# Performance work log

Hardware: AMD Instinct MI355X
Metric: run time of the kernel (lower is better)

## Reference

```python
import jax, jax.numpy as jnp
import numpy as np

N_NODES = 100000
N_EDGES = 1000000
IN_FEATS = 64
HID = 128
NUM_CLASSES = 10


def setup_inputs() -> dict:
    key = jax.random.key(0)
    ks = jax.random.split(key, 8)
    x = jax.random.normal(ks[0], (N_NODES, IN_FEATS), dtype=jnp.float32)
    edge_index = jax.random.randint(ks[1], (2, N_EDGES), 0, N_NODES, dtype=jnp.int64)
    # Glorot-style init scale for weights
    def w(k, fan_in, fan_out):
        s = (2.0 / (fan_in + fan_out)) ** 0.5
        return jax.random.normal(k, (fan_in, fan_out), dtype=jnp.float32) * s
    return {
        "x": x,
        "edge_index": edge_index,
        "W1": w(ks[2], IN_FEATS, HID),
        "b1": jnp.zeros((HID,), dtype=jnp.float32),
        "W2": w(ks[3], HID, HID),
        "b2": jnp.zeros((HID,), dtype=jnp.float32),
        "Wl": w(ks[4], HID, NUM_CLASSES),
        "bl": jnp.zeros((NUM_CLASSES,), dtype=jnp.float32),
    }


def _gcn_conv(x, src, dst, norm, W, b, num_nodes):
    # PyG GCNConv: h = x W, then out_i = sum_{j->i} norm_ij * h_j + b
    h = x @ W  # [N, out]
    msgs = h[src] * norm[:, None]  # gather + scale  [E+N, out]
    out = jax.ops.segment_sum(msgs, dst, num_segments=num_nodes)
    return out + b


def reference(x, edge_index, W1, b1, W2, b2, Wl, bl):
    N = x.shape[0]
    loops = jnp.arange(N, dtype=edge_index.dtype)
    src = jnp.concatenate([edge_index[0], loops])  # source nodes (messages from)
    dst = jnp.concatenate([edge_index[1], loops])  # target nodes (aggregate at)
    # symmetric normalization: deg over targets (includes self-loops)
    deg = jax.ops.segment_sum(jnp.ones(dst.shape, dtype=x.dtype), dst, num_segments=N)
    dinv = jnp.where(deg > 0, jax.lax.rsqrt(deg), 0.0)
    norm = dinv[src] * dinv[dst]  # [E+N]

    h = jax.nn.relu(_gcn_conv(x, src, dst, norm, W1, b1, N))
    h = jax.nn.relu(_gcn_conv(h, src, dst, norm, W2, b2, N))
    return jax.nn.log_softmax(h @ Wl + bl, axis=1)
```

## Files before the change

kernel.cpp:

```cpp
#include <hip/hip_runtime.h>
#include <hip/hip_fp16.h>
#include <math.h>

#define NUM_CLASSES 10

#define BSH 7
#define BSZ 128
#define BCAP 1792
#define NBMAX 1024
#define P1BATCH 4096

typedef _Float16 half8  __attribute__((ext_vector_type(8)));
typedef _Float16 half4t __attribute__((ext_vector_type(4)));
typedef float    floatx4 __attribute__((ext_vector_type(4)));

__global__ __launch_bounds__(256) void prep_kernel(const float* __restrict__ W1,
                                                   const float* __restrict__ W2,
                                                   const float* __restrict__ Wlc,
                                                   _Float16* __restrict__ W1t,
                                                   _Float16* __restrict__ W2t,
                                                   _Float16* __restrict__ Wct,
                                                   int* __restrict__ fill, int nbuck) {
    const int b = blockIdx.x, tid = threadIdx.x;
    if (b == 0) {
        for (int i = tid; i < nbuck; i += 256) fill[i] = 0;
    }
    if (b < 32) {
        int i = b * 256 + tid;
        int k = i >> 7, c = i & 127;
        W1t[c * 72 + k] = (_Float16)W1[i];
    } else if (b < 96) {
        int i = (b - 32) * 256 + tid;
        int k = i >> 7, c = i & 127;
        W2t[c * 136 + k] = (_Float16)W2[i];
    } else {
        for (int i = tid; i < 16 * 136; i += 256) {
            int c = i / 136, k = i - c * 136;
            float v = (c < NUM_CLASSES && k < 128) ? Wlc[k * NUM_CLASSES + c] : 0.0f;
            Wct[i] = (_Float16)v;
        }
    }
}

__global__ __launch_bounds__(256) void csr_p1_kernel(const int* __restrict__ src,
                                                     const int* __restrict__ dst,
                                                     int* __restrict__ bucket_fill,
                                                     unsigned* __restrict__ pairs, int E) {
    __shared__ int hist[NBMAX], base[NBMAX], cur[NBMAX];
    const int tid = threadIdx.x;
    for (int i = tid; i < NBMAX; i += 256) { hist[i] = 0; cur[i] = 0; }
    __syncthreads();
    const int bb = blockIdx.x * P1BATCH;
    unsigned pk[16];
    int bk[16];
    int cnt = 0;
#pragma unroll
    for (int i = 0; i < 16; ++i) {
        int idx = bb + i * 256 + tid;
        if (idx < E) {
            int s = src[idx], d = dst[idx];
            bk[i] = d >> BSH;
            pk[i] = ((unsigned)s << BSH) | (unsigned)(d & (BSZ - 1));
            atomicAdd(&hist[bk[i]], 1);
            cnt = i + 1;
        }
    }
    __syncthreads();
    for (int i = tid; i < NBMAX; i += 256)
        if (hist[i] > 0) base[i] = atomicAdd(&bucket_fill[i], hist[i]);
    __syncthreads();
#pragma unroll
    for (int i = 0; i < 16; ++i) {
        if (i < cnt) {
            int b = bk[i];
            int r = atomicAdd(&cur[b], 1) + base[b];
            if (r < BCAP) pairs[(size_t)b * BCAP + r] = pk[i];
        }
    }
}

__global__ __launch_bounds__(256) void scan_base_kernel(const int* __restrict__ fill,
                                                        int* __restrict__ bbase, int nbuck) {
    __shared__ int s1[256];
    const int tid = threadIdx.x;
    const int i0 = tid * 4;
    int v[4];
#pragma unroll
    for (int j = 0; j < 4; ++j) v[j] = (i0 + j < nbuck) ? fill[i0 + j] : 0;
    int t = v[0] + v[1] + v[2] + v[3];
    s1[tid] = t;
    __syncthreads();
    for (int off = 1; off < 256; off <<= 1) {
        int u = (tid >= off) ? s1[tid - off] : 0;
        __syncthreads();
        s1[tid] += u;
        __syncthreads();
    }
    int run = s1[tid] - t;
#pragma unroll
    for (int j = 0; j < 4; ++j) {
        if (i0 + j < nbuck) { bbase[i0 + j] = run; run += v[j]; }
    }
    if (tid == 255) bbase[nbuck] = s1[255];
}

__global__ __launch_bounds__(256) void csr_p2_kernel(const int* __restrict__ bucket_fill,
                                                     const int* __restrict__ bucket_base,
                                                     const unsigned* __restrict__ pairs,
                                                     const float* __restrict__ x,
                                                     int* __restrict__ rowstart,
                                                     float* __restrict__ dinv,
                                                     int* __restrict__ csr_src,
                                                     __half2* __restrict__ xs_h,
                                                     int N, int nbuck) {
    __shared__ int cnt[BSZ], excl[BSZ], cur[BSZ];
    __shared__ int s1[BSZ];
    const int tid = threadIdx.x;
    const int b = blockIdx.x;
    const int node0 = b << BSH;
    const int nodes_b = min(BSZ, N - node0);

    if (tid < BSZ) { cnt[tid] = 0; cur[tid] = 0; }
    __syncthreads();
    const int bbase = bucket_base[b];
    const int ne = bucket_fill[b];

    const unsigned* bp = pairs + (size_t)b * BCAP;
    for (int i = tid; i < ne; i += 256)
        atomicAdd(&cnt[bp[i] & (BSZ - 1)], 1);
    __syncthreads();
    int c = (tid < BSZ) ? cnt[tid] : 0;
    if (tid < BSZ) s1[tid] = c;
    __syncthreads();
    for (int off = 1; off < BSZ; off <<= 1) {
        int t = (tid < BSZ && tid >= off) ? s1[tid - off] : 0;
        __syncthreads();
        if (tid < BSZ) s1[tid] += t;
        __syncthreads();
    }
    if (tid < BSZ) excl[tid] = s1[tid] - c;
    __syncthreads();

    if (tid < nodes_b) {
        rowstart[node0 + tid] = bbase + excl[tid];
        dinv[node0 + tid] = rsqrtf((float)cnt[tid] + 1.0f);
    }
    if (b == nbuck - 1 && tid == 0) rowstart[N] = bbase + ne;

    for (int i = tid; i < nodes_b * 32; i += 256) {
        int ln = i >> 5;
        float d = rsqrtf((float)cnt[ln] + 1.0f);
        float2 v = ((const float2*)x)[(size_t)node0 * 32 + i];
        xs_h[(size_t)node0 * 32 + i] = __floats2half2_rn(v.x * d, v.y * d);
    }
    for (int i = tid; i < ne; i += 256) {
        unsigned p = bp[i];
        int d = (int)(p & (BSZ - 1));
        int r = atomicAdd(&cur[d], 1);
        csr_src[bbase + excl[d] + r] = (int)(p >> BSH);
    }
}

template <int F>
__global__ __launch_bounds__(256) void gather_h_kernel(const __half2* __restrict__ hs,
                                                       const float* __restrict__ dinv,
                                                       const int* __restrict__ rowstart,
                                                       const int* __restrict__ csr_src,
                                                       __half2* __restrict__ out, int N) {
    constexpr int F2 = F / 2;
    int node = (blockIdx.x * 256 + threadIdx.x) >> 6;
    int lane = threadIdx.x & 63;
    if (node >= N) return;
    int f2 = lane & (F2 - 1);

    int beg = rowstart[node];
    int end = rowstart[node + 1];
    int deg = end - beg;

    float2 self = __half22float2(hs[(size_t)node * F2 + f2]);
    float2 acc;

    if (deg <= 16) {
        int myidx = (lane < deg) ? csr_src[beg + lane] : node;
        float comp = (float)(deg - 15);
        acc.x = self.x * comp;
        acc.y = self.y * comp;
        float2 v[16];
#pragma unroll
        for (int u = 0; u < 16; ++u) {
            int s = __shfl(myidx, u);
            v[u] = __half22float2(hs[(size_t)s * F2 + f2]);
        }
#pragma unroll
        for (int u = 0; u < 16; ++u) { acc.x += v[u].x; acc.y += v[u].y; }
    } else {
        int lim = deg < 64 ? deg : 64;
        int myidx = (lane < lim) ? csr_src[beg + lane] : node;
        int itersUp = (lim + 7) & ~7;
        float comp = (float)(1 - (itersUp - lim));
        acc.x = self.x * comp;
        acc.y = self.y * comp;
        for (int j = 0; j < itersUp; j += 8) {
            int s[8];
#pragma unroll
            for (int u = 0; u < 8; ++u) s[u] = __shfl(myidx, j + u);
            float2 v[8];
#pragma unroll
            for (int u = 0; u < 8; ++u) v[u] = __half22float2(hs[(size_t)s[u] * F2 + f2]);
#pragma unroll
            for (int u = 0; u < 8; ++u) { acc.x += v[u].x; acc.y += v[u].y; }
        }
        for (int j = beg + 64; j < end; ++j) {
            int s = csr_src[j];
            float2 v = __half22float2(hs[(size_t)s * F2 + f2]);
            acc.x += v.x;
            acc.y += v.y;
        }
    }

    if (F == 128 || lane < 32) {
        float d = dinv[node];
        out[(size_t)node * F2 + f2] = __floats2half2_rn(d * acc.x, d * acc.y);
    }
}

template <int K, bool SCALE_OUT>
__global__ __launch_bounds__(256) void gemm_mfma_kernel(const _Float16* __restrict__ In,
                                                        const _Float16* __restrict__ Wt,
                                                        const float* __restrict__ bias,
                                                        const float* __restrict__ dinv,
                                                        _Float16* __restrict__ Out, int N) {
    constexpr int KP = K + 8;
    constexpr int NC = K / 32;
    __shared__ _Float16 Wl[128 * KP];
    __shared__ float bias_s[128];
    const int tid = threadIdx.x;

    for (int i = tid; i < (128 * KP) / 8; i += 256)
        ((floatx4*)Wl)[i] = ((const floatx4*)Wt)[i];
    if (tid < 128) bias_s[tid] = bias[tid];
    __syncthreads();

    const int lane = tid & 63;
    const int wave = tid >> 6;
    const int q = lane >> 4;
    const int l15 = lane & 15;

#pragma unroll
    for (int iter = 0; iter < 2; ++iter) {
        int myrow = blockIdx.x * 128 + iter * 64 + wave * 16 + l15;
        int r = myrow < N ? myrow : N - 1;
        half8 xf[NC];
#pragma unroll
        for (int c = 0; c < NC; ++c)
            xf[c] = *(const half8*)(In + (size_t)r * K + c * 32 + q * 8);
        floatx4 acc[8];
#pragma unroll
        for (int t = 0; t < 8; ++t) acc[t] = (floatx4){0.f, 0.f, 0.f, 0.f};
#pragma unroll
        for (int c = 0; c < NC; ++c) {
#pragma unroll
            for (int t = 0; t < 8; ++t) {
                half8 wf = *(const half8*)(Wl + (t * 16 + l15) * KP + c * 32 + q * 8);
                acc[t] = __builtin_amdgcn_mfma_f32_16x16x32_f16(wf, xf[c], acc[t], 0, 0, 0);
            }
        }
        if (myrow < N) {
            float sc = SCALE_OUT ? dinv[myrow] : 1.0f;
#pragma unroll
            for (int t = 0; t < 8; ++t) {
                int c0 = t * 16 + q * 4;
                floatx4 bv = *(const floatx4*)&bias_s[c0];
                half4t h;
#pragma unroll
                for (int j = 0; j < 4; ++j)
                    h[j] = (_Float16)(sc * fmaxf(acc[t][j] + bv[j], 0.0f));
                *(half4t*)(Out + (size_t)myrow * 128 + c0) = h;
            }
        }
    }
}

__global__ __launch_bounds__(256) void gemm_final_kernel(const _Float16* __restrict__ In,
                                                         const _Float16* __restrict__ Wt,
                                                         const float* __restrict__ bias,
                                                         const _Float16* __restrict__ Wct,
                                                         const float* __restrict__ bl,
                                                         float* __restrict__ out, int N) {
    constexpr int K = 128, KP = 136, NC = 4;
    __shared__ _Float16 Wl[128 * KP];
    __shared__ _Float16 Wc[16 * KP];
    __shared__ float bias_s[128];
    __shared__ float bl_s[16];
    __shared__ _Float16 act_s[4][16 * KP];
    const int tid = threadIdx.x;

    for (int i = tid; i < (128 * KP) / 8; i += 256)
        ((floatx4*)Wl)[i] = ((const floatx4*)Wt)[i];
    for (int i = tid; i < (16 * KP) / 8; i += 256)
        ((floatx4*)Wc)[i] = ((const floatx4*)Wct)[i];
    if (tid < 128) bias_s[tid] = bias[tid];
    if (tid < 16) bl_s[tid] = (tid < NUM_CLASSES) ? bl[tid] : -1e30f;
    __syncthreads();

    const int lane = tid & 63;
    const int wave = tid >> 6;
    const int q = lane >> 4;
    const int l15 = lane & 15;
    _Float16* As = act_s[wave];

    half8 wcf[NC];
#pragma unroll
    for (int c = 0; c < NC; ++c)
        wcf[c] = *(const half8*)(Wc + l15 * KP + c * 32 + q * 8);
    float myclsb[4];
#pragma unroll
    for (int reg = 0; reg < 4; ++reg) myclsb[reg] = bl_s[q * 4 + reg];

#pragma unroll
    for (int iter = 0; iter < 2; ++iter) {
        int rowbase = blockIdx.x * 128 + iter * 64 + wave * 16;
        int myrow = rowbase + l15;
        int r = myrow < N ? myrow : N - 1;
        half8 xf[NC];
#pragma unroll
        for (int c = 0; c < NC; ++c)
            xf[c] = *(const half8*)(In + (size_t)r * K + c * 32 + q * 8);
        floatx4 acc[8];
#pragma unroll
        for (int t = 0; t < 8; ++t) acc[t] = (floatx4){0.f, 0.f, 0.f, 0.f};
#pragma unroll
        for (int c = 0; c < NC; ++c) {
#pragma unroll
            for (int t = 0; t < 8; ++t) {
                half8 wf = *(const half8*)(Wl + (t * 16 + l15) * KP + c * 32 + q * 8);
                acc[t] = __builtin_amdgcn_mfma_f32_16x16x32_f16(wf, xf[c], acc[t], 0, 0, 0);
            }
        }
#pragma unroll
        for (int t = 0; t < 8; ++t) {
            int c0 = t * 16 + q * 4;
            floatx4 bv = *(const floatx4*)&bias_s[c0];
            half4t h;
#pragma unroll
            for (int j = 0; j < 4; ++j)
                h[j] = (_Float16)fmaxf(acc[t][j] + bv[j], 0.0f);
            *(half4t*)&As[l15 * KP + c0] = h;
        }
        floatx4 lg = (floatx4){0.f, 0.f, 0.f, 0.f};
#pragma unroll
        for (int c = 0; c < NC; ++c) {
            half8 af = *(const half8*)(As + l15 * KP + c * 32 + q * 8);
            lg = __builtin_amdgcn_mfma_f32_16x16x32_f16(wcf[c], af, lg, 0, 0, 0);
        }
        if (myrow < N) {
            float v[4];
#pragma unroll
            for (int reg = 0; reg < 4; ++reg) v[reg] = lg[reg] + myclsb[reg];
            float mx = fmaxf(fmaxf(v[0], v[1]), fmaxf(v[2], v[3]));
            mx = fmaxf(mx, __shfl_xor(mx, 16));
            mx = fmaxf(mx, __shfl_xor(mx, 32));
            float sm = expf(v[0] - mx) + expf(v[1] - mx) + expf(v[2] - mx) + expf(v[3] - mx);
            sm += __shfl_xor(sm, 16);
            sm += __shfl_xor(sm, 32);
            float lse = mx + logf(sm);
#pragma unroll
            for (int reg = 0; reg < 4; ++reg) {
                int cls = q * 4 + reg;
                if (cls < NUM_CLASSES)
                    out[(size_t)myrow * NUM_CLASSES + cls] = v[reg] - lse;
            }
        }
    }
}

extern "C" void kernel_launch(void* const* d_in, const int* in_sizes, int n_in,
                              void* d_out, int out_size, void* d_ws, size_t ws_size,
                              hipStream_t stream) {
    const float* x  = (const float*)d_in[0];
    const int*   ei = (const int*)d_in[1];
    const float* W1 = (const float*)d_in[2];
    const float* b1 = (const float*)d_in[3];
    const float* W2 = (const float*)d_in[4];
    const float* b2 = (const float*)d_in[5];
    const float* Wlc = (const float*)d_in[6];
    const float* bl = (const float*)d_in[7];
    float* out = (float*)d_out;

    const int N = in_sizes[0] / 64;
    const int E = in_sizes[1] / 2;
    const int* src = ei;
    const int* dst = ei + E;
    const int nbuck = (N + BSZ - 1) >> BSH;

    char* ws = (char*)d_ws;
    int*      bucket_fill = (int*)(ws + 0);
    int*      rowstart    = (int*)(ws + 4096);
    float*    dinv        = (float*)(ws + 524288);
    _Float16* W1t         = (_Float16*)(ws + 1048576);
    _Float16* W2t         = (_Float16*)(ws + 1069056);
    _Float16* Wct         = (_Float16*)(ws + 1103872);
    int*      bucket_base = (int*)(ws + 1110016);
    unsigned* pairs       = (unsigned*)(ws + 2097152);
    int*      csr_src     = (int*)(ws + 12582912);
    char*     region1     = ws + 16777216;
    char*     region2     = ws + 68157440;
    __half2*  xs_h = (__half2*)region1;
    __half2*  g1h  = (__half2*)(region1 + 13631488);
    __half2*  g2h  = (__half2*)region1;
    __half2*  a1_h = (__half2*)region2;

    const int P1B = (E + P1BATCH - 1) / P1BATCH;
    const int GB  = (N + 127) / 128;
    const int WVB = (N + 3) / 4;

    prep_kernel<<<97, 256, 0, stream>>>(W1, W2, Wlc, W1t, W2t, Wct, bucket_fill, nbuck);
    csr_p1_kernel<<<P1B, 256, 0, stream>>>(src, dst, bucket_fill, pairs, E);
    scan_base_kernel<<<1, 256, 0, stream>>>(bucket_fill, bucket_base, nbuck);
    csr_p2_kernel<<<nbuck, 256, 0, stream>>>(bucket_fill, bucket_base, pairs, x, rowstart,
                                             dinv, csr_src, xs_h, N, nbuck);

    gather_h_kernel<64><<<WVB, 256, 0, stream>>>(xs_h, dinv, rowstart, csr_src, g1h, N);
    gemm_mfma_kernel<64, true><<<GB, 256, 0, stream>>>((const _Float16*)g1h, W1t, b1, dinv,
                                                       (_Float16*)a1_h, N);

    gather_h_kernel<128><<<WVB, 256, 0, stream>>>(a1_h, dinv, rowstart, csr_src, g2h, N);
    gemm_final_kernel<<<GB, 256, 0, stream>>>((const _Float16*)g2h, W2t, b2, Wct, bl, out, N);
}
```

Measured before the change: 226.0 us.

## Fuse neighbor gathers into GEMM kernels and fold bucket scan into CSR pass

Each gather-aggregate pass is merged into the following MFMA GEMM kernel, so aggregated rows go into shared memory instead of making a round trip through global memory. The separate single-block bucket scan is removed; each csr_p2 block now sums the fills of all preceding buckets itself with a block reduction. This drops two intermediate buffers and three launches. In exchange, gather latency and the GEMM now serialize within a block, and the second fused kernel uses 64-row tiles, so the weight loads into shared memory are repeated twice as often.

Measured after the change: 290.4 us. 1.29x slower.

```diff
diff --git a/kernel.cpp b/kernel.cpp
--- a/kernel.cpp
+++ b/kernel.cpp
@@ -79,33 +79,7 @@
     }
 }
 
-__global__ __launch_bounds__(256) void scan_base_kernel(const int* __restrict__ fill,
-                                                        int* __restrict__ bbase, int nbuck) {
-    __shared__ int s1[256];
-    const int tid = threadIdx.x;
-    const int i0 = tid * 4;
-    int v[4];
-#pragma unroll
-    for (int j = 0; j < 4; ++j) v[j] = (i0 + j < nbuck) ? fill[i0 + j] : 0;
-    int t = v[0] + v[1] + v[2] + v[3];
-    s1[tid] = t;
-    __syncthreads();
-    for (int off = 1; off < 256; off <<= 1) {
-        int u = (tid >= off) ? s1[tid - off] : 0;
-        __syncthreads();
-        s1[tid] += u;
-        __syncthreads();
-    }
-    int run = s1[tid] - t;
-#pragma unroll
-    for (int j = 0; j < 4; ++j) {
-        if (i0 + j < nbuck) { bbase[i0 + j] = run; run += v[j]; }
-    }
-    if (tid == 255) bbase[nbuck] = s1[255];
-}
-
 __global__ __launch_bounds__(256) void csr_p2_kernel(const int* __restrict__ bucket_fill,
-                                                     const int* __restrict__ bucket_base,
                                                      const unsigned* __restrict__ pairs,
                                                      const float* __restrict__ x,
                                                      int* __restrict__ rowstart,
@@ -114,16 +88,24 @@
                                                      __half2* __restrict__ xs_h,
                                                      int N, int nbuck) {
     __shared__ int cnt[BSZ], excl[BSZ], cur[BSZ];
-    __shared__ int s1[BSZ];
+    __shared__ int s1[256];
     const int tid = threadIdx.x;
     const int b = blockIdx.x;
     const int node0 = b << BSH;
     const int nodes_b = min(BSZ, N - node0);
 
     if (tid < BSZ) { cnt[tid] = 0; cur[tid] = 0; }
-    __syncthreads();
-    const int bbase = bucket_base[b];
+    int part = 0;
+    for (int j = tid; j < b; j += 256) part += bucket_fill[j];
+    s1[tid] = part;
+    __syncthreads();
+    for (int off = 128; off > 0; off >>= 1) {
+        if (tid < off) s1[tid] += s1[tid + off];
+        __syncthreads();
+    }
+    const int bbase = s1[0];
     const int ne = bucket_fill[b];
+    __syncthreads();
 
     const unsigned* bp = pairs + (size_t)b * BCAP;
     for (int i = tid; i < ne; i += 256)
@@ -161,99 +143,90 @@
     }
 }
 
-template <int F>
-__global__ __launch_bounds__(256) void gather_h_kernel(const __half2* __restrict__ hs,
-                                                       const float* __restrict__ dinv,
-                                                       const int* __restrict__ rowstart,
-                                                       const int* __restrict__ csr_src,
-                                                       __half2* __restrict__ out, int N) {
-    constexpr int F2 = F / 2;
-    int node = (blockIdx.x * 256 + threadIdx.x) >> 6;
-    int lane = threadIdx.x & 63;
-    if (node >= N) return;
-    int f2 = lane & (F2 - 1);
-
-    int beg = rowstart[node];
-    int end = rowstart[node + 1];
-    int deg = end - beg;
-
-    float2 self = __half22float2(hs[(size_t)node * F2 + f2]);
-    float2 acc;
-
-    if (deg <= 16) {
-        int myidx = (lane < deg) ? csr_src[beg + lane] : node;
-        float comp = (float)(deg - 15);
-        acc.x = self.x * comp;
-        acc.y = self.y * comp;
-        float2 v[16];
-#pragma unroll
-        for (int u = 0; u < 16; ++u) {
-            int s = __shfl(myidx, u);
-            v[u] = __half22float2(hs[(size_t)s * F2 + f2]);
-        }
-#pragma unroll
-        for (int u = 0; u < 16; ++u) { acc.x += v[u].x; acc.y += v[u].y; }
-    } else {
-        int lim = deg < 64 ? deg : 64;
-        int myidx = (lane < lim) ? csr_src[beg + lane] : node;
-        int itersUp = (lim + 7) & ~7;
-        float comp = (float)(1 - (itersUp - lim));
-        acc.x = self.x * comp;
-        acc.y = self.y * comp;
-        for (int j = 0; j < itersUp; j += 8) {
-            int s[8];
-#pragma unroll
-            for (int u = 0; u < 8; ++u) s[u] = __shfl(myidx, j + u);
-            float2 v[8];
-#pragma unroll
-            for (int u = 0; u < 8; ++u) v[u] = __half22float2(hs[(size_t)s[u] * F2 + f2]);
-#pragma unroll
-            for (int u = 0; u < 8; ++u) { acc.x += v[u].x; acc.y += v[u].y; }
-        }
-        for (int j = beg + 64; j < end; ++j) {
-            int s = csr_src[j];
-            float2 v = __half22float2(hs[(size_t)s * F2 + f2]);
-            acc.x += v.x;
-            acc.y += v.y;
-        }
-    }
-
-    if (F == 128 || lane < 32) {
-        float d = dinv[node];
-        out[(size_t)node * F2 + f2] = __floats2half2_rn(d * acc.x, d * acc.y);
-    }
-}
-
-template <int K, bool SCALE_OUT>
-__global__ __launch_bounds__(256) void gemm_mfma_kernel(const _Float16* __restrict__ In,
-                                                        const _Float16* __restrict__ Wt,
-                                                        const float* __restrict__ bias,
-                                                        const float* __restrict__ dinv,
-                                                        _Float16* __restrict__ Out, int N) {
-    constexpr int KP = K + 8;
-    constexpr int NC = K / 32;
+__global__ __launch_bounds__(256) void fused_gemm1_kernel(const __half2* __restrict__ xs,
+                                                          const float* __restrict__ dinv,
+                                                          const int* __restrict__ rowstart,
+                                                          const int* __restrict__ csr_src,
+                                                          const _Float16* __restrict__ Wt,
+                                                          const float* __restrict__ bias,
+                                                          _Float16* __restrict__ Out, int N) {
+    constexpr int KP = 72, NC = 2;
     __shared__ _Float16 Wl[128 * KP];
+    __shared__ _Float16 acts[128 * KP];
     __shared__ float bias_s[128];
     const int tid = threadIdx.x;
 
     for (int i = tid; i < (128 * KP) / 8; i += 256)
         ((floatx4*)Wl)[i] = ((const floatx4*)Wt)[i];
     if (tid < 128) bias_s[tid] = bias[tid];
-    __syncthreads();
 
     const int lane = tid & 63;
     const int wave = tid >> 6;
+    const int row0 = blockIdx.x * 128;
+    const int f2 = lane & 31;
+
+    for (int i = 0; i < 32; ++i) {
+        int r = wave * 32 + i;
+        int node = row0 + r;
+        float2 acc = make_float2(0.f, 0.f);
+        if (node < N) {
+            int beg = rowstart[node], end = rowstart[node + 1], deg = end - beg;
+            float2 self = __half22float2(xs[(size_t)node * 32 + f2]);
+            if (deg <= 16) {
+                int myidx = (lane < deg) ? csr_src[beg + lane] : node;
+                float comp = (float)(deg - 15);
+                acc.x = self.x * comp;
+                acc.y = self.y * comp;
+                float2 v[16];
+#pragma unroll
+                for (int u = 0; u < 16; ++u) {
+                    int s = __shfl(myidx, u);
+                    v[u] = __half22float2(xs[(size_t)s * 32 + f2]);
+                }
+#pragma unroll
+                for (int u = 0; u < 16; ++u) { acc.x += v[u].x; acc.y += v[u].y; }
+            } else {
+                int lim = deg < 64 ? deg : 64;
+                int myidx = (lane < lim) ? csr_src[beg + lane] : node;
+                int itersUp = (lim + 7) & ~7;
+                float comp = (float)(1 - (itersUp - lim));
+                acc.x = self.x * comp;
+                acc.y = self.y * comp;
+                for (int j = 0; j < itersUp; j += 8) {
+                    int s[8];
+#pragma unroll
+                    for (int u = 0; u < 8; ++u) s[u] = __shfl(myidx, j + u);
+                    float2 v[8];
+#pragma unroll
+                    for (int u = 0; u < 8; ++u) v[u] = __half22float2(xs[(size_t)s[u] * 32 + f2]);
+#pragma unroll
+                    for (int u = 0; u < 8; ++u) { acc.x += v[u].x; acc.y += v[u].y; }
+                }
+                for (int j = beg + 64; j < end; ++j) {
+                    float2 v = __half22float2(xs[(size_t)csr_src[j] * 32 + f2]);
+                    acc.x += v.x;
+                    acc.y += v.y;
+                }
+            }
+            float d = dinv[node];
+            acc.x *= d;
+            acc.y *= d;
+        }
+        if (lane < 32)
+            *(__half2*)&acts[r * KP + 2 * f2] = __floats2half2_rn(acc.x, acc.y);
+    }
+    __syncthreads();
+
     const int q = lane >> 4;
     const int l15 = lane & 15;
-
 #pragma unroll
     for (int iter = 0; iter < 2; ++iter) {
-        int myrow = blockIdx.x * 128 + iter * 64 + wave * 16 + l15;
-        int r = myrow < N ? myrow : N - 1;
+        int lrow = iter * 64 + wave * 16 + l15;
+        int myrow = row0 + lrow;
         half8 xf[NC];
 #pragma unroll
         for (int c = 0; c < NC; ++c)
-            xf[c] = *(const half8*)(In + (size_t)r * K + c * 32 + q * 8);
+            xf[c] = *(const half8*)(acts + lrow * KP + c * 32 + q * 8);
         floatx4 acc[8];
 #pragma unroll
         for (int t = 0; t < 8; ++t) acc[t] = (floatx4){0.f, 0.f, 0.f, 0.f};
@@ -266,7 +239,7 @@
             }
         }
         if (myrow < N) {
-            float sc = SCALE_OUT ? dinv[myrow] : 1.0f;
+            float sc = dinv[myrow];
 #pragma unroll
             for (int t = 0; t < 8; ++t) {
                 int c0 = t * 16 + q * 4;
@@ -281,18 +254,21 @@
     }
 }
 
-__global__ __launch_bounds__(256) void gemm_final_kernel(const _Float16* __restrict__ In,
-                                                         const _Float16* __restrict__ Wt,
-                                                         const float* __restrict__ bias,
-                                                         const _Float16* __restrict__ Wct,
-                                                         const float* __restrict__ bl,
-                                                         float* __restrict__ out, int N) {
-    constexpr int K = 128, KP = 136, NC = 4;
+__global__ __launch_bounds__(256) void fused_final_kernel(const __half2* __restrict__ a1,
+                                                          const float* __restrict__ dinv,
+                                                          const int* __restrict__ rowstart,
+                                                          const int* __restrict__ csr_src,
+                                                          const _Float16* __restrict__ Wt,
+                                                          const float* __restrict__ bias,
+                                                          const _Float16* __restrict__ Wct,
+                                                          const float* __restrict__ bl,
+                                                          float* __restrict__ out, int N) {
+    constexpr int KP = 136, NC = 4;
     __shared__ _Float16 Wl[128 * KP];
+    __shared__ _Float16 acts[64 * KP];
     __shared__ _Float16 Wc[16 * KP];
     __shared__ float bias_s[128];
     __shared__ float bl_s[16];
-    __shared__ _Float16 act_s[4][16 * KP];
     const int tid = threadIdx.x;
 
     for (int i = tid; i < (128 * KP) / 8; i += 256)
@@ -301,14 +277,64 @@
         ((floatx4*)Wc)[i] = ((const floatx4*)Wct)[i];
     if (tid < 128) bias_s[tid] = bias[tid];
     if (tid < 16) bl_s[tid] = (tid < NUM_CLASSES) ? bl[tid] : -1e30f;
-    __syncthreads();
 
     const int lane = tid & 63;
     const int wave = tid >> 6;
+    const int row0 = blockIdx.x * 64;
+
+    for (int i = 0; i < 16; ++i) {
+        int r = wave * 16 + i;
+        int node = row0 + r;
+        float2 acc = make_float2(0.f, 0.f);
+        if (node < N) {
+            int beg = rowstart[node], end = rowstart[node + 1], deg = end - beg;
+            float2 self = __half22float2(a1[(size_t)node * 64 + lane]);
+            if (deg <= 16) {
+                int myidx = (lane < deg) ? csr_src[beg + lane] : node;
+                float comp = (float)(deg - 15);
+                acc.x = self.x * comp;
+                acc.y = self.y * comp;
+                float2 v[16];
+#pragma unroll
+                for (int u = 0; u < 16; ++u) {
+                    int s = __shfl(myidx, u);
+                    v[u] = __half22float2(a1[(size_t)s * 64 + lane]);
+                }
+#pragma unroll
+                for (int u = 0; u < 16; ++u) { acc.x += v[u].x; acc.y += v[u].y; }
+            } else {
+                int lim = deg < 64 ? deg : 64;
+                int myidx = (lane < lim) ? csr_src[beg + lane] : node;
+                int itersUp = (lim + 7) & ~7;
+                float comp = (float)(1 - (itersUp - lim));
+                acc.x = self.x * comp;
+                acc.y = self.y * comp;
+                for (int j = 0; j < itersUp; j += 8) {
+                    int s[8];
+#pragma unroll
+                    for (int u = 0; u < 8; ++u) s[u] = __shfl(myidx, j + u);
+                    float2 v[8];
+#pragma unroll
+                    for (int u = 0; u < 8; ++u) v[u] = __half22float2(a1[(size_t)s[u] * 64 + lane]);
+#pragma unroll
+                    for (int u = 0; u < 8; ++u) { acc.x += v[u].x; acc.y += v[u].y; }
+                }
+                for (int j = beg + 64; j < end; ++j) {
+                    float2 v = __half22float2(a1[(size_t)csr_src[j] * 64 + lane]);
+                    acc.x += v.x;
+                    acc.y += v.y;
+                }
+            }
+            float d = dinv[node];
+            acc.x *= d;
+            acc.y *= d;
+        }
+        *(__half2*)&acts[r * KP + 2 * lane] = __floats2half2_rn(acc.x, acc.y);
+    }
+    __syncthreads();
+
     const int q = lane >> 4;
     const int l15 = lane & 15;
-    _Float16* As = act_s[wave];
-
     half8 wcf[NC];
 #pragma unroll
     for (int c = 0; c < NC; ++c)
@@ -317,59 +343,55 @@
 #pragma unroll
     for (int reg = 0; reg < 4; ++reg) myclsb[reg] = bl_s[q * 4 + reg];
 
-#pragma unroll
-    for (int iter = 0; iter < 2; ++iter) {
-        int rowbase = blockIdx.x * 128 + iter * 64 + wave * 16;
-        int myrow = rowbase + l15;
-        int r = myrow < N ? myrow : N - 1;
-        half8 xf[NC];
-#pragma unroll
-        for (int c = 0; c < NC; ++c)
-            xf[c] = *(const half8*)(In + (size_t)r * K + c * 32 + q * 8);
-        floatx4 acc[8];
-#pragma unroll
-        for (int t = 0; t < 8; ++t) acc[t] = (floatx4){0.f, 0.f, 0.f, 0.f};
-#pragma unroll
-        for (int c = 0; c < NC; ++c) {
-#pragma unroll
-            for (int t = 0; t < 8; ++t) {
-                half8 wf = *(const half8*)(Wl + (t * 16 + l15) * KP + c * 32 + q * 8);
-                acc[t] = __builtin_amdgcn_mfma_f32_16x16x32_f16(wf, xf[c], acc[t], 0, 0, 0);
-            }
-        }
+    const int lrow = wave * 16 + l15;
+    const int myrow = row0 + lrow;
+    half8 xf[NC];
+#pragma unroll
+    for (int c = 0; c < NC; ++c)
+        xf[c] = *(const half8*)(acts + lrow * KP + c * 32 + q * 8);
+    floatx4 acc[8];
+#pragma unroll
+    for (int t = 0; t < 8; ++t) acc[t] = (floatx4){0.f, 0.f, 0.f, 0.f};
+#pragma unroll
+    for (int c = 0; c < NC; ++c) {
 #pragma unroll
         for (int t = 0; t < 8; ++t) {
-            int c0 = t * 16 + q * 4;
-            floatx4 bv = *(const floatx4*)&bias_s[c0];
-            half4t h;
-#pragma unroll
-            for (int j = 0; j < 4; ++j)
-                h[j] = (_Float16)fmaxf(acc[t][j] + bv[j], 0.0f);
-            *(half4t*)&As[l15 * KP + c0] = h;
-        }
-        floatx4 lg = (floatx4){0.f, 0.f, 0.f, 0.f};
-#pragma unroll
-        for (int c = 0; c < NC; ++c) {
-            half8 af = *(const half8*)(As + l15 * KP + c * 32 + q * 8);
-            lg = __builtin_amdgcn_mfma_f32_16x16x32_f16(wcf[c], af, lg, 0, 0, 0);
-        }
-        if (myrow < N) {
-            float v[4];
-#pragma unroll
-            for (int reg = 0; reg < 4; ++reg) v[reg] = lg[reg] + myclsb[reg];
-            float mx = fmaxf(fmaxf(v[0], v[1]), fmaxf(v[2], v[3]));
-            mx = fmaxf(mx, __shfl_xor(mx, 16));
-            mx = fmaxf(mx, __shfl_xor(mx, 32));
-            float sm = expf(v[0] - mx) + expf(v[1] - mx) + expf(v[2] - mx) + expf(v[3] - mx);
-            sm += __shfl_xor(sm, 16);
-            sm += __shfl_xor(sm, 32);
-            float lse = mx + logf(sm);
-#pragma unroll
-            for (int reg = 0; reg < 4; ++reg) {
-                int cls = q * 4 + reg;
-                if (cls < NUM_CLASSES)
-                    out[(size_t)myrow * NUM_CLASSES + cls] = v[reg] - lse;
-            }
+            half8 wf = *(const half8*)(Wl + (t * 16 + l15) * KP + c * 32 + q * 8);
+            acc[t] = __builtin_amdgcn_mfma_f32_16x16x32_f16(wf, xf[c], acc[t], 0, 0, 0);
+        }
+    }
+#pragma unroll
+    for (int t = 0; t < 8; ++t) {
+        int c0 = t * 16 + q * 4;
+        floatx4 bv = *(const floatx4*)&bias_s[c0];
+        half4t h;
+#pragma unroll
+        for (int j = 0; j < 4; ++j)
+            h[j] = (_Float16)fmaxf(acc[t][j] + bv[j], 0.0f);
+        *(half4t*)&acts[lrow * KP + c0] = h;
+    }
+    floatx4 lg = (floatx4){0.f, 0.f, 0.f, 0.f};
+#pragma unroll
+    for (int c = 0; c < NC; ++c) {
+        half8 af = *(const half8*)(acts + lrow * KP + c * 32 + q * 8);
+        lg = __builtin_amdgcn_mfma_f32_16x16x32_f16(wcf[c], af, lg, 0, 0, 0);
+    }
+    if (myrow < N) {
+        float v[4];
+#pragma unroll
+        for (int reg = 0; reg < 4; ++reg) v[reg] = lg[reg] + myclsb[reg];
+        float mx = fmaxf(fmaxf(v[0], v[1]), fmaxf(v[2], v[3]));
+        mx = fmaxf(mx, __shfl_xor(mx, 16));
+        mx = fmaxf(mx, __shfl_xor(mx, 32));
+        float sm = expf(v[0] - mx) + expf(v[1] - mx) + expf(v[2] - mx) + expf(v[3] - mx);
+        sm += __shfl_xor(sm, 16);
+        sm += __shfl_xor(sm, 32);
+        float lse = mx + logf(sm);
+#pragma unroll
+        for (int reg = 0; reg < 4; ++reg) {
+            int cls = q * 4 + reg;
+            if (cls < NUM_CLASSES)
+                out[(size_t)myrow * NUM_CLASSES + cls] = v[reg] - lse;
         }
     }
 }
@@ -400,30 +422,23 @@
     _Float16* W1t         = (_Float16*)(ws + 1048576);
     _Float16* W2t         = (_Float16*)(ws + 1069056);
     _Float16* Wct         = (_Float16*)(ws + 1103872);
-    int*      bucket_base = (int*)(ws + 1110016);
     unsigned* pairs       = (unsigned*)(ws + 2097152);
     int*      csr_src     = (int*)(ws + 12582912);
-    char*     region1     = ws + 16777216;
-    char*     region2     = ws + 68157440;
-    __half2*  xs_h = (__half2*)region1;
-    __half2*  g1h  = (__half2*)(region1 + 13631488);
-    __half2*  g2h  = (__half2*)region1;
-    __half2*  a1_h = (__half2*)region2;
+    __half2*  xs_h        = (__half2*)(ws + 16777216);
+    __half2*  a1_h        = (__half2*)(ws + 68157440);
 
     const int P1B = (E + P1BATCH - 1) / P1BATCH;
-    const int GB  = (N + 127) / 128;
-    const int WVB = (N + 3) / 4;
+    const int G1B = (N + 127) / 128;
+    const int G2B = (N + 63) / 64;
 
     prep_kernel<<<97, 256, 0, stream>>>(W1, W2, Wlc, W1t, W2t, Wct, bucket_fill, nbuck);
     csr_p1_kernel<<<P1B, 256, 0, stream>>>(src, dst, bucket_fill, pairs, E);
-    scan_base_kernel<<<1, 256, 0, stream>>>(bucket_fill, bucket_base, nbuck);
-    csr_p2_kernel<<<nbuck, 256, 0, stream>>>(bucket_fill, bucket_base, pairs, x, rowstart,
-                                             dinv, csr_src, xs_h, N, nbuck);
-
-    gather_h_kernel<64><<<WVB, 256, 0, stream>>>(xs_h, dinv, rowstart, csr_src, g1h, N);
-    gemm_mfma_kernel<64, true><<<GB, 256, 0, stream>>>((const _Float16*)g1h, W1t, b1, dinv,
-                                                       (_Float16*)a1_h, N);
-
-    gather_h_kernel<128><<<WVB, 256, 0, stream>>>(a1_h, dinv, rowstart, csr_src, g2h, N);
-    gemm_final_kernel<<<GB, 256, 0, stream>>>((const _Float16*)g2h, W2t, b2, Wct, bl, out, N);
-}
+    csr_p2_kernel<<<nbuck, 256, 0, stream>>>(bucket_fill, pairs, x, rowstart, dinv,
+                                             csr_src, xs_h, N, nbuck);
+
+    fused_gemm1_kernel<<<G1B, 256, 0, stream>>>(xs_h, dinv, rowstart, csr_src,
+                                                W1t, b1, (_Float16*)a1_h, N);
+
+    fused_final_kernel<<<G2B, 256, 0, stream>>>(a1_h, dinv, rowstart, csr_src,
+                                                W2t, b2, Wct, bl, out, N);
+}
```
